# Kernel optimization log

Hardware: AMD Instinct MI355X
Metric: run time of the kernel (lower is better)

The kernel has to match this reference:

```python
import jax, jax.numpy as jnp
import numpy as np

B, T, C = 4, 2048, 2048
H = 16
D = C // H  # 128


def setup_inputs() -> dict:
    key = jax.random.key(0)
    k1, k2, k3, k4 = jax.random.split(key, 4)
    x = jax.random.normal(k1, (B, T, C), dtype=jnp.float32)
    rope_freqs = jax.random.uniform(k2, (D // 2,), dtype=jnp.float32)
    # torch Linear weights: (out_features, in_features)
    W_attn = jax.random.normal(k3, (3 * C, C), dtype=jnp.float32) * (1.0 / np.sqrt(C))
    W_proj = jax.random.normal(k4, (C, C), dtype=jnp.float32) * (1.0 / np.sqrt(C))
    return {"x": x, "rope_freqs": rope_freqs, "W_attn": W_attn, "W_proj": W_proj}


def _apply_rope(q, k, rope_freqs):
    # q, k: (B, H, T, D); rope_freqs: (D//2,)
    S = q.shape[2]
    positions = jnp.arange(S, dtype=q.dtype)[:, None]            # (S, 1)
    theta = positions * rope_freqs[None, :]                       # (S, D//2)
    sin_t = jnp.sin(theta)[None, None]                            # (1,1,S,D//2)
    cos_t = jnp.cos(theta)[None, None]
    q1, q2 = q[..., 0::2], q[..., 1::2]
    k1, k2 = k[..., 0::2], k[..., 1::2]
    q_out = jnp.concatenate([q1 * cos_t - q2 * sin_t, q1 * sin_t + q2 * cos_t], axis=-1)
    k_out = jnp.concatenate([k1 * cos_t - k2 * sin_t, k1 * sin_t + k2 * cos_t], axis=-1)
    return q_out, k_out


def reference(x, rope_freqs, W_attn, W_proj):
    b, t, c = x.shape
    qkv = jnp.einsum('btc,fc->btf', x, W_attn)                    # (B,T,3C)
    q, k, v = jnp.split(qkv, 3, axis=-1)
    q = q.reshape(b, t, H, D).transpose(0, 2, 1, 3)               # (B,H,T,D)
    k = k.reshape(b, t, H, D).transpose(0, 2, 1, 3)
    v = v.reshape(b, t, H, D).transpose(0, 2, 1, 3)
    q, k = _apply_rope(q, k, rope_freqs)
    scale = 1.0 / jnp.sqrt(jnp.asarray(D, dtype=x.dtype))
    scores = jnp.einsum('bhqd,bhkd->bhqk', q, k) * scale          # (B,H,T,T)
    causal = jnp.tril(jnp.ones((t, t), dtype=bool))
    scores = jnp.where(causal[None, None], scores, jnp.asarray(-jnp.inf, dtype=scores.dtype))
    probs = jax.nn.softmax(scores, axis=-1)
    y = jnp.einsum('bhqk,bhkd->bhqd', probs, v)                   # (B,H,T,D)
    y = y.transpose(0, 2, 1, 3).reshape(b, t, c)
    return jnp.einsum('btc,fc->btf', y, W_proj)
```

## Files before the change

kernel.cpp:

```cpp
#include <hip/hip_runtime.h>
#include <cstdint>
#include <cstddef>


typedef unsigned short u16;
typedef u16    u16x8 __attribute__((ext_vector_type(8)));
typedef __bf16 bf16x8 __attribute__((ext_vector_type(8)));
typedef float  f32x4 __attribute__((ext_vector_type(4)));

#define MFMA16(a, b, c) __builtin_amdgcn_mfma_f32_16x16x32_bf16( \
    __builtin_bit_cast(bf16x8, (a)), __builtin_bit_cast(bf16x8, (b)), (c), 0, 0, 0)

static __device__ __forceinline__ u16 f2b(float f) {
  unsigned u = __builtin_bit_cast(unsigned, f);
  unsigned r = (u + 0x7FFFu + ((u >> 16) & 1u)) >> 16;
  return (u16)r;
}

static __device__ __forceinline__ void gld_lds16(const void* g, void* l) {
  __builtin_amdgcn_global_load_lds(
      (__attribute__((address_space(1))) unsigned int*)(void*)(g),
      (__attribute__((address_space(3))) unsigned int*)(l),
      16, 0, 0);
}

#define BARRIER() asm volatile("s_barrier" ::: "memory")
#define LGKM0()   do { asm volatile("s_waitcnt lgkmcnt(0)" ::: "memory"); \
                       __builtin_amdgcn_sched_barrier(0); } while (0)
#define WAIT_VM(n) asm volatile("s_waitcnt vmcnt(" #n ")" ::: "memory")

__global__ __launch_bounds__(256) void cvt_bf16(const float4* __restrict__ src,
                                                u16x8* __restrict__ dst, int n8) {
  int i = blockIdx.x * 256 + threadIdx.x;
  if (i >= n8) return;
  float4 a = src[i * 2], b = src[i * 2 + 1];
  u16x8 o;
  o[0] = f2b(a.x); o[1] = f2b(a.y); o[2] = f2b(a.z); o[3] = f2b(a.w);
  o[4] = f2b(b.x); o[5] = f2b(b.y); o[6] = f2b(b.z); o[7] = f2b(b.w);
  dst[i] = o;
}

static __device__ __forceinline__ void rdA(u16x8 (&af)[4][2], const u16* p,
                                           int cx0, int cx1) {
#pragma unroll
  for (int i = 0; i < 4; ++i) {
    af[i][0] = *(const u16x8*)(p + i * 1024 + cx0);
    af[i][1] = *(const u16x8*)(p + i * 1024 + cx1);
  }
}

static __device__ __forceinline__ void rdB(u16x8 (&bf)[2][2], const u16* p,
                                           int cx0, int cx1) {
#pragma unroll
  for (int j = 0; j < 2; ++j) {
    bf[j][0] = *(const u16x8*)(p + j * 1024 + cx0);
    bf[j][1] = *(const u16x8*)(p + j * 1024 + cx1);
  }
}

static __device__ __forceinline__ void mm16(f32x4 (&acc)[8][4], int ib, int jb,
                                            const u16x8 (&af)[4][2],
                                            const u16x8 (&bf)[2][2]) {
#pragma unroll
  for (int i = 0; i < 4; ++i)
#pragma unroll
    for (int j = 0; j < 2; ++j) {
      acc[ib + i][jb + j] = MFMA16(af[i][0], bf[j][0], acc[ib + i][jb + j]);
      acc[ib + i][jb + j] = MFMA16(af[i][1], bf[j][1], acc[ib + i][jb + j]);
    }
}

static __device__ __forceinline__ void gemm256_main(
    const u16* __restrict__ A, const u16* __restrict__ Bw, int K,
    int m0, int n0, u16* sm, f32x4 (&acc)[8][4]) {
  const int tid = threadIdx.x;
  const int lane = tid & 63, wv = tid >> 6;
  const int quad = lane >> 4, col = lane & 15;
  const int wm = wv >> 2, wn = wv & 3;

  u16* LA0 = sm;
  u16* LB0 = sm + 16384;
  u16* LA1 = sm + 32768;
  u16* LB1 = sm + 49152;

#pragma unroll
  for (int i = 0; i < 8; ++i)
#pragma unroll
    for (int j = 0; j < 4; ++j) acc[i][j] = (f32x4){0.f, 0.f, 0.f, 0.f};

  const int r8 = lane >> 3, ch = lane & 7;
  const int sc8 = (ch ^ r8) << 3;
  const u16 *aS[4], *bS[4];
  int dof[4];
#pragma unroll
  for (int u = 0; u < 4; ++u) {
    int row = u * 64 + wv * 8 + r8;
    aS[u] = A + (size_t)(m0 + row) * K + sc8;
    bS[u] = Bw + (size_t)(n0 + row) * K + sc8;
    dof[u] = (u * 64 + wv * 8) * 64;
  }

  const int cx0 = ((quad) ^ (col & 7)) << 3;
  const int cx1 = ((4 | quad) ^ (col & 7)) << 3;
  const int offA = (wm * 128 + col) * 64;
  const int offB = (wn * 64 + col) * 64;

  gld_lds16(bS[0], LB0 + dof[0]); gld_lds16(bS[1], LB0 + dof[1]);
  gld_lds16(bS[2], LB0 + dof[2]); gld_lds16(bS[3], LB0 + dof[3]);
  gld_lds16(aS[0], LA0 + dof[0]); gld_lds16(aS[2], LA0 + dof[2]);
  gld_lds16(aS[1], LA0 + dof[1]); gld_lds16(aS[3], LA0 + dof[3]);
  WAIT_VM(2);
  BARRIER();

  u16x8 af[4][2], bfL[2][2], bfH[2][2];
  const int nIt = K >> 7;
#pragma unroll 1
  for (int it = 0; it < nIt; ++it) {
    const size_t ko = (size_t)it * 128 + 64;
    const size_t kn = (size_t)it * 128 + 128;
    const bool hn = (it + 1 < nIt);

    rdA(af, LA0 + offA, cx0, cx1);
    rdB(bfL, LB0 + offB, cx0, cx1);
    gld_lds16(bS[0] + ko, LB1 + dof[0]); gld_lds16(bS[1] + ko, LB1 + dof[1]);
    BARRIER(); LGKM0();
    __builtin_amdgcn_s_setprio(1); mm16(acc, 0, 0, af, bfL);
    __builtin_amdgcn_s_setprio(0);
    BARRIER();
    rdB(bfH, LB0 + offB + 2048, cx0, cx1);
    gld_lds16(bS[2] + ko, LB1 + dof[2]); gld_lds16(bS[3] + ko, LB1 + dof[3]);
    WAIT_VM(4);
    BARRIER(); LGKM0();
    __builtin_amdgcn_s_setprio(1); mm16(acc, 0, 2, af, bfH);
    __builtin_amdgcn_s_setprio(0);
    BARRIER();
    rdA(af, LA0 + offA + 4096, cx0, cx1);
    gld_lds16(aS[0] + ko, LA1 + dof[0]); gld_lds16(aS[2] + ko, LA1 + dof[2]);
    BARRIER(); LGKM0();
    __builtin_amdgcn_s_setprio(1); mm16(acc, 4, 0, af, bfL);
    __builtin_amdgcn_s_setprio(0);
    BARRIER();
    gld_lds16(aS[1] + ko, LA1 + dof[1]); gld_lds16(aS[3] + ko, LA1 + dof[3]);
    WAIT_VM(2);
    BARRIER(); __builtin_amdgcn_sched_barrier(0);
    __builtin_amdgcn_s_setprio(1); mm16(acc, 4, 2, af, bfH);
    __builtin_amdgcn_s_setprio(0);
    BARRIER();
    rdA(af, LA1 + offA, cx0, cx1);
    rdB(bfL, LB1 + offB, cx0, cx1);
    if (hn) { gld_lds16(bS[0] + kn, LB0 + dof[0]); gld_lds16(bS[1] + kn, LB0 + dof[1]); }
    BARRIER(); LGKM0();
    __builtin_amdgcn_s_setprio(1); mm16(acc, 0, 0, af, bfL);
    __builtin_amdgcn_s_setprio(0);
    BARRIER();
    rdB(bfH, LB1 + offB + 2048, cx0, cx1);
    if (hn) {
      gld_lds16(bS[2] + kn, LB0 + dof[2]); gld_lds16(bS[3] + kn, LB0 + dof[3]);
      WAIT_VM(4);
    } else {
      WAIT_VM(0);
    }
    BARRIER(); LGKM0();
    __builtin_amdgcn_s_setprio(1); mm16(acc, 0, 2, af, bfH);
    __builtin_amdgcn_s_setprio(0);
    BARRIER();
    rdA(af, LA1 + offA + 4096, cx0, cx1);
    if (hn) { gld_lds16(aS[0] + kn, LA0 + dof[0]); gld_lds16(aS[2] + kn, LA0 + dof[2]); }
    BARRIER(); LGKM0();
    __builtin_amdgcn_s_setprio(1); mm16(acc, 4, 0, af, bfL);
    __builtin_amdgcn_s_setprio(0);
    BARRIER();
    if (hn) { gld_lds16(aS[1] + kn, LA0 + dof[1]); gld_lds16(aS[3] + kn, LA0 + dof[3]); }
    WAIT_VM(2);
    BARRIER(); __builtin_amdgcn_sched_barrier(0);
    __builtin_amdgcn_s_setprio(1); mm16(acc, 4, 2, af, bfH);
    __builtin_amdgcn_s_setprio(0);
    BARRIER();
  }
}

__global__ __launch_bounds__(512, 2) void gemm_qkv(
    const u16* __restrict__ A, const u16* __restrict__ Bw,
    const float* __restrict__ freqs, int K,
    u16* __restrict__ Qp, u16* __restrict__ Kp, u16* __restrict__ Vp) {
  extern __shared__ u16 sm[];
  const int m0 = blockIdx.y * 256, n0 = blockIdx.x * 256;
  f32x4 acc[8][4];
  gemm256_main(A, Bw, K, m0, n0, sm, acc);

  const int tid = threadIdx.x;
  const int lane = tid & 63, wv = tid >> 6;
  const int quad = lane >> 4, col = lane & 15;
  const int wm = wv >> 2, wn = wv & 3;

  const int which = n0 >> 11;
  if (which == 2) {
#pragma unroll
    for (int i = 0; i < 8; ++i) {
      int mg = m0 + wm * 128 + i * 16 + quad * 4;
#pragma unroll
      for (int j = 0; j < 4; ++j) {
        int vcol = (n0 + wn * 64 + j * 16 + col) & 2047;
        int h = vcol >> 7, d = vcol & 127;
#pragma unroll
        for (int r = 0; r < 4; ++r) {
          int m = mg + r;
          int b = m >> 11, t = m & 2047;
          size_t off = ((((size_t)(b * 16 + h)) * 32 + (size_t)(t >> 6)) * 128 + (size_t)d) * 64
                       + (size_t)(t & 63);
          Vp[off] = f2b(acc[i][j][r]);
        }
      }
    }
  } else {
    u16* dst = (which == 0) ? Qp : Kp;
#pragma unroll
    for (int j = 0; j < 4; ++j) {
      int ncol = (n0 + wn * 64 + j * 16 + col) & 2047;
      int h = ncol >> 7, dd = ncol & 127;
      int jj = dd >> 1;
      bool even = (dd & 1) == 0;
      float fr = freqs[jj];
      int dout = even ? jj : jj + 64;
#pragma unroll
      for (int i = 0; i < 8; ++i) {
        int mg = m0 + wm * 128 + i * 16 + quad * 4;
#pragma unroll
        for (int r = 0; r < 4; ++r) {
          float own = acc[i][j][r];
          float par = __shfl_xor(own, 1);
          int m = mg + r;
          int b = m >> 11, t = m & 2047;
          float theta = (float)t * fr;
          float rev = theta * 0.15915494309189535f;
          rev -= floorf(rev);
          float s = __builtin_amdgcn_sinf(rev);
          float c = __builtin_amdgcn_cosf(rev);
          float outv = even ? (own * c - par * s) : (par * s + own * c);
          size_t off = ((((size_t)(b * 16 + h)) << 11 | (size_t)t) << 7) | (size_t)dout;
          dst[off] = f2b(outv);
        }
      }
    }
  }
}

__global__ __launch_bounds__(512, 2) void gemm_proj(
    const u16* __restrict__ A, const u16* __restrict__ Bw,
    int N, int K, float* __restrict__ out) {
  extern __shared__ u16 sm[];
  const int m0 = blockIdx.y * 256, n0 = blockIdx.x * 256;
  f32x4 acc[8][4];
  gemm256_main(A, Bw, K, m0, n0, sm, acc);

  const int tid = threadIdx.x;
  const int lane = tid & 63, wv = tid >> 6;
  const int quad = lane >> 4, col = lane & 15;
  const int wm = wv >> 2, wn = wv & 3;

#pragma unroll
  for (int i = 0; i < 8; ++i) {
    int mg = m0 + wm * 128 + i * 16 + quad * 4;
#pragma unroll
    for (int j = 0; j < 4; ++j) {
      int ng = n0 + wn * 64 + j * 16 + col;
#pragma unroll
      for (int r = 0; r < 4; ++r) out[(size_t)(mg + r) * N + ng] = acc[i][j][r];
    }
  }
}

__global__ __launch_bounds__(512, 4) void fattn(
    const u16* __restrict__ Qb, const u16* __restrict__ Kb, const u16* __restrict__ Vt,
    u16* __restrict__ Yb) {
  __shared__ alignas(16) u16 lK[64 * 128];
  __shared__ alignas(16) u16 lVt[128 * 64];
  __shared__ alignas(16) u16 lP[8][16 * 64];

  const int tid = threadIdx.x;
  const int lane = tid & 63, wv = tid >> 6;
  const int quad = lane >> 4, col = lane & 15;
  const int bh = blockIdx.x;
  const int p = blockIdx.y;
  const int b = bh >> 4, h = bh & 15;
  const size_t base = (size_t)bh << 18;
  const float kcomb = 0.08838834764831845f * 1.4426950408889634f;

#pragma unroll 1
  for (int phase = 0; phase < 2; ++phase) {
    const int tq = phase ? (15 - p) : p;
    const int qr0 = tq * 128 + wv * 16;
    const int dkt = qr0 >> 6;

    u16x8 qf[4];
#pragma unroll
    for (int t = 0; t < 4; ++t)
      qf[t] = *(const u16x8*)(Qb + base + (size_t)(qr0 + col) * 128 + t * 32 + quad * 8);

    f32x4 mrow = (f32x4){-1e30f, -1e30f, -1e30f, -1e30f};
    f32x4 lrow = (f32x4){0.f, 0.f, 0.f, 0.f};
    f32x4 o[8];
#pragma unroll
    for (int dt = 0; dt < 8; ++dt) o[dt] = (f32x4){0.f, 0.f, 0.f, 0.f};

    const int nkt = 2 * tq + 2;
#pragma unroll 1
    for (int kt = 0; kt < nkt; ++kt) {
      __syncthreads();
      if (wv < 4) {
#pragma unroll
        for (int u = 0; u < 4; ++u) {
          int row = wv * 16 + u * 4 + (lane >> 4);
          int sc = (lane & 15) ^ (row & 15);
          gld_lds16(Kb + base + (size_t)(kt * 64 + row) * 128 + (sc << 3),
                    lK + (size_t)(wv * 16 + u * 4) * 128);
        }
      } else {
        int vw = wv - 4;
        const u16* vbase = Vt + ((size_t)(bh * 32 + kt) << 13);
#pragma unroll
        for (int u = 0; u < 4; ++u) {
          int row = vw * 32 + u * 8 + (lane >> 3);
          int sc = (lane & 7) ^ (row & 7);
          gld_lds16(vbase + (size_t)row * 64 + (sc << 3),
                    lVt + (size_t)(vw * 32 + u * 8) * 64);
        }
      }
      __syncthreads();

      if (kt <= dkt) {
        f32x4 sv[4];
#pragma unroll
        for (int nt = 0; nt < 4; ++nt) {
          f32x4 s = (f32x4){0.f, 0.f, 0.f, 0.f};
#pragma unroll
          for (int t = 0; t < 4; ++t) {
            int krow = nt * 16 + col;
            u16x8 kf = *(const u16x8*)&lK[krow * 128 + ((((t << 2) | quad) ^ (krow & 15)) << 3)];
            s = MFMA16(qf[t], kf, s);
          }
          sv[nt] = s;
        }
#pragma unroll
        for (int nt = 0; nt < 4; ++nt)
#pragma unroll
          for (int r = 0; r < 4; ++r) sv[nt][r] *= kcomb;
        if (kt == dkt) {
#pragma unroll
          for (int nt = 0; nt < 4; ++nt) {
            int cg = kt * 64 + nt * 16 + col;
#pragma unroll
            for (int r = 0; r < 4; ++r)
              if (cg > qr0 + quad * 4 + r) sv[nt][r] = -1e30f;
          }
        }
        f32x4 mx = sv[0];
#pragma unroll
        for (int nt = 1; nt < 4; ++nt)
#pragma unroll
          for (int r = 0; r < 4; ++r) mx[r] = fmaxf(mx[r], sv[nt][r]);
#pragma unroll
        for (int off = 1; off < 16; off <<= 1)
#pragma unroll
          for (int r = 0; r < 4; ++r) mx[r] = fmaxf(mx[r], __shfl_xor(mx[r], off));
        f32x4 alpha;
#pragma unroll
        for (int r = 0; r < 4; ++r) {
          float mn = fmaxf(mrow[r], mx[r]);
          alpha[r] = exp2f(mrow[r] - mn);
          mrow[r] = mn;
        }
        f32x4 ps = (f32x4){0.f, 0.f, 0.f, 0.f};
#pragma unroll
        for (int nt = 0; nt < 4; ++nt)
#pragma unroll
          for (int r = 0; r < 4; ++r) {
            float pe = exp2f(sv[nt][r] - mrow[r]);
            ps[r] += pe;
            int row = quad * 4 + r;
            int ch = ((nt << 1) | (col >> 3)) ^ (row & 7);
            lP[wv][row * 64 + (ch << 3) + (col & 7)] = f2b(pe);
          }
#pragma unroll
        for (int off = 1; off < 16; off <<= 1)
#pragma unroll
          for (int r = 0; r < 4; ++r) ps[r] += __shfl_xor(ps[r], off);
#pragma unroll
        for (int r = 0; r < 4; ++r) lrow[r] = lrow[r] * alpha[r] + ps[r];
#pragma unroll
        for (int dt = 0; dt < 8; ++dt)
#pragma unroll
          for (int r = 0; r < 4; ++r) o[dt][r] *= alpha[r];
#pragma unroll
        for (int t = 0; t < 2; ++t) {
          u16x8 pf = *(const u16x8*)&lP[wv][col * 64 + ((((t << 2) | quad) ^ (col & 7)) << 3)];
#pragma unroll
          for (int dt = 0; dt < 8; ++dt) {
            int drow = dt * 16 + col;
            u16x8 vf = *(const u16x8*)&lVt[drow * 64 + ((((t << 2) | quad) ^ (drow & 7)) << 3)];
            o[dt] = MFMA16(pf, vf, o[dt]);
          }
        }
      }
    }

    f32x4 inv;
#pragma unroll
    for (int r = 0; r < 4; ++r) inv[r] = 1.0f / lrow[r];
#pragma unroll
    for (int dt = 0; dt < 8; ++dt)
#pragma unroll
      for (int r = 0; r < 4; ++r) {
        float y = o[dt][r] * inv[r];
        int q = qr0 + quad * 4 + r;
        Yb[((size_t)(b * 2048 + q)) * 2048 + h * 128 + dt * 16 + col] = f2b(y);
      }
  }
}

extern "C" void kernel_launch(void* const* d_in, const int* in_sizes, int n_in,
                              void* d_out, int out_size, void* d_ws, size_t ws_size,
                              hipStream_t stream) {
  (void)in_sizes; (void)n_in; (void)out_size; (void)ws_size;
  const float* x     = (const float*)d_in[0];
  const float* freqs = (const float*)d_in[1];
  const float* Wattn = (const float*)d_in[2];
  const float* Wproj = (const float*)d_in[3];
  float* out = (float*)d_out;
  char* ws = (char*)d_ws;

  u16* Wq_b = (u16*)(ws + 0);
  u16* Wp_b = (u16*)(ws + 25165824);
  u16* x_b  = (u16*)(ws + 33554432);
  u16* Qb   = (u16*)(ws + 67108864);
  u16* Kb   = (u16*)(ws + 100663296);
  u16* Vt   = (u16*)(ws + 134217728);
  u16* Yb   = (u16*)(ws + 167772160);

  static bool attr_done = false;
  if (!attr_done) {
    (void)hipFuncSetAttribute((const void*)gemm_qkv,
                              hipFuncAttributeMaxDynamicSharedMemorySize, 131072);
    (void)hipFuncSetAttribute((const void*)gemm_proj,
                              hipFuncAttributeMaxDynamicSharedMemorySize, 131072);
    attr_done = true;
  }

  cvt_bf16<<<6144, 256, 0, stream>>>((const float4*)Wattn, (u16x8*)Wq_b, 12582912 / 8);
  cvt_bf16<<<2048, 256, 0, stream>>>((const float4*)Wproj, (u16x8*)Wp_b, 4194304 / 8);
  cvt_bf16<<<8192, 256, 0, stream>>>((const float4*)x, (u16x8*)x_b, 16777216 / 8);

  gemm_qkv<<<dim3(24, 32), 512, 131072, stream>>>(x_b, Wq_b, freqs, 2048, Qb, Kb, Vt);
  fattn<<<dim3(64, 8), 512, 0, stream>>>(Qb, Kb, Vt, Yb);
  gemm_proj<<<dim3(8, 32), 512, 131072, stream>>>(Yb, Wp_b, 2048, 2048, out);
}
```

Before: 591.0 us.

## Stage GEMM epilogues through LDS, remap block order, double-buffer attention K/V loads

The QKV GEMM epilogue now writes RoPE'd Q/K and transposed V tiles into swizzled LDS and then stores them with coalesced 16-byte global writes, in place of scattered 2-byte stores. Both GEMMs use a 1D grid with a remapped block order, likely to improve L2 reuse across the XCDs. Flash attention double-buffers its K/V tiles in dynamic LDS so the next tile's loads overlap compute. In exchange it uses more LDS and adds barriers, which may lower attention occupancy.

```diff
diff --git a/kernel.cpp b/kernel.cpp
--- a/kernel.cpp
+++ b/kernel.cpp
@@ -184,7 +184,12 @@
     const float* __restrict__ freqs, int K,
     u16* __restrict__ Qp, u16* __restrict__ Kp, u16* __restrict__ Vp) {
   extern __shared__ u16 sm[];
-  const int m0 = blockIdx.y * 256, n0 = blockIdx.x * 256;
+  const int bid = blockIdx.x;
+  const int x = bid & 7, o = bid >> 3;
+  const int rnd = o >> 5, w = o & 31;
+  const int m0 = (x * 4 + (w & 3)) * 256;
+  const int n0 = (rnd * 8 + (w >> 2)) * 256;
+
   f32x4 acc[8][4];
   gemm256_main(A, Bw, K, m0, n0, sm, acc);
 
@@ -194,53 +199,86 @@
   const int wm = wv >> 2, wn = wv & 3;
 
   const int which = n0 >> 11;
+  const int h0 = (n0 & 2047) >> 7;
+  const int b = m0 >> 11, t0 = m0 & 2047;
+  const int hl = wn >> 1;
+
+  __syncthreads();
+
   if (which == 2) {
 #pragma unroll
-    for (int i = 0; i < 8; ++i) {
-      int mg = m0 + wm * 128 + i * 16 + quad * 4;
-#pragma unroll
-      for (int j = 0; j < 4; ++j) {
-        int vcol = (n0 + wn * 64 + j * 16 + col) & 2047;
-        int h = vcol >> 7, d = vcol & 127;
+    for (int j = 0; j < 4; ++j) {
+      int d = (wn & 1) * 64 + j * 16 + col;
+      int key = (d >> 1) & 7;
+#pragma unroll
+      for (int i = 0; i < 8; ++i)
 #pragma unroll
         for (int r = 0; r < 4; ++r) {
-          int m = mg + r;
-          int b = m >> 11, t = m & 2047;
-          size_t off = ((((size_t)(b * 16 + h)) * 32 + (size_t)(t >> 6)) * 128 + (size_t)d) * 64
-                       + (size_t)(t & 63);
-          Vp[off] = f2b(acc[i][j][r]);
+          int tgl = wm * 128 + i * 16 + quad * 4 + r;
+          int reg = hl * 4 + (tgl >> 6);
+          int tc = tgl & 63;
+          sm[reg * 8192 + d * 64 + (((tc >> 3) ^ key) << 3) + (tc & 7)] =
+              f2b(acc[i][j][r]);
         }
-      }
+    }
+    __syncthreads();
+#pragma unroll
+    for (int s = 0; s < 16; ++s) {
+      int cch = tid + (s << 9);
+      int reg = cch >> 10, ci = cch & 1023;
+      int d = ci >> 3, cc = ci & 7;
+      u16x8 v = *(const u16x8*)(sm + reg * 8192 + d * 64 +
+                                (((cc ^ ((d >> 1) & 7))) << 3));
+      int hh = reg >> 2, ktg = reg & 3;
+      int kt = (t0 >> 6) + ktg;
+      size_t off = (((size_t)((b * 16 + h0 + hh) * 32 + kt)) << 13) +
+                   (size_t)d * 64 + (cc << 3);
+      *(u16x8*)(Vp + off) = v;
     }
   } else {
     u16* dst = (which == 0) ? Qp : Kp;
+    const bool evenlane = (col & 1) == 0;
+    const int rlo = evenlane ? 0 : 2;
 #pragma unroll
     for (int j = 0; j < 4; ++j) {
-      int ncol = (n0 + wn * 64 + j * 16 + col) & 2047;
-      int h = ncol >> 7, dd = ncol & 127;
+      int dd = (wn & 1) * 64 + j * 16 + col;
       int jj = dd >> 1;
-      bool even = (dd & 1) == 0;
       float fr = freqs[jj];
-      int dout = even ? jj : jj + 64;
 #pragma unroll
       for (int i = 0; i < 8; ++i) {
-        int mg = m0 + wm * 128 + i * 16 + quad * 4;
-#pragma unroll
-        for (int r = 0; r < 4; ++r) {
-          float own = acc[i][j][r];
-          float par = __shfl_xor(own, 1);
-          int m = mg + r;
-          int b = m >> 11, t = m & 2047;
+        float oth[4];
+#pragma unroll
+        for (int r = 0; r < 4; ++r) oth[r] = __shfl_xor(acc[i][j][r], 1);
+#pragma unroll
+        for (int rr = 0; rr < 2; ++rr) {
+          int r = rlo + rr;
+          float q1 = evenlane ? acc[i][j][r] : oth[r];
+          float q2 = evenlane ? oth[r] : acc[i][j][r];
+          int tgl = wm * 128 + i * 16 + quad * 4 + r;
+          int t = t0 + tgl;
           float theta = (float)t * fr;
           float rev = theta * 0.15915494309189535f;
           rev -= floorf(rev);
-          float s = __builtin_amdgcn_sinf(rev);
-          float c = __builtin_amdgcn_cosf(rev);
-          float outv = even ? (own * c - par * s) : (par * s + own * c);
-          size_t off = ((((size_t)(b * 16 + h)) << 11 | (size_t)t) << 7) | (size_t)dout;
-          dst[off] = f2b(outv);
+          float sn = __builtin_amdgcn_sinf(rev);
+          float cs = __builtin_amdgcn_cosf(rev);
+          unsigned pk = (unsigned)f2b(q1 * cs - q2 * sn) |
+                        ((unsigned)f2b(q1 * sn + q2 * cs) << 16);
+          int row = hl * 256 + tgl;
+          int sc = (jj >> 2) ^ (row & 15);
+          *(unsigned*)(sm + row * 128 + (sc << 3) + 2 * (jj & 3)) = pk;
         }
       }
+    }
+    __syncthreads();
+#pragma unroll
+    for (int s = 0; s < 16; ++s) {
+      int cch = tid + (s << 9);
+      int row = cch >> 4, cc = cch & 15;
+      u16x8 v = *(const u16x8*)(sm + row * 128 + ((cc ^ (row & 15)) << 3));
+      int hh = row >> 8, tl = row & 255;
+      size_t off = ((size_t)((b * 16 + h0 + hh) * 2048 + t0 + tl)) * 128 +
+                   (cc << 3);
+      *(u16x8*)(dst + off) = v;
     }
   }
 }
@@ -249,7 +287,11 @@
     const u16* __restrict__ A, const u16* __restrict__ Bw,
     int N, int K, float* __restrict__ out) {
   extern __shared__ u16 sm[];
-  const int m0 = blockIdx.y * 256, n0 = blockIdx.x * 256;
+  const int bid = blockIdx.x;
+  const int x = bid & 7, w = bid >> 3;
+  const int m0 = (x * 4 + (w & 3)) * 256;
+  const int n0 = (w >> 2) * 256;
+
   f32x4 acc[8][4];
   gemm256_main(A, Bw, K, m0, n0, sm, acc);
 
@@ -273,9 +315,8 @@
 __global__ __launch_bounds__(512, 4) void fattn(
     const u16* __restrict__ Qb, const u16* __restrict__ Kb, const u16* __restrict__ Vt,
     u16* __restrict__ Yb) {
-  __shared__ alignas(16) u16 lK[64 * 128];
-  __shared__ alignas(16) u16 lVt[128 * 64];
-  __shared__ alignas(16) u16 lP[8][16 * 64];
+  extern __shared__ u16 smem[];
+  u16* lP = smem + 32768 + (threadIdx.x >> 6) * 1024;
 
   const int tid = threadIdx.x;
   const int lane = tid & 63, wv = tid >> 6;
@@ -304,31 +345,50 @@
     for (int dt = 0; dt < 8; ++dt) o[dt] = (f32x4){0.f, 0.f, 0.f, 0.f};
 
     const int nkt = 2 * tq + 2;
+
+#define FA_STAGE(KT, BI)                                                        \
+    do {                                                                        \
+      if (wv < 4) {                                                             \
+        u16* lkd = smem + (BI) * 8192;                                          \
+        _Pragma("unroll")                                                       \
+        for (int u = 0; u < 4; ++u) {                                           \
+          int row = wv * 16 + u * 4 + (lane >> 4);                              \
+          int sc = (lane & 15) ^ (row & 15);                                    \
+          gld_lds16(Kb + base + (size_t)((KT) * 64 + row) * 128 + (sc << 3),    \
+                    lkd + (size_t)(wv * 16 + u * 4) * 128);                     \
+        }                                                                       \
+      } else {                                                                  \
+        int vw = wv - 4;                                                        \
+        u16* lvd = smem + 16384 + (BI) * 8192;                                  \
+        const u16* vbase = Vt + ((size_t)(bh * 32 + (KT)) << 13);               \
+        _Pragma("unroll")                                                       \
+        for (int u = 0; u < 4; ++u) {                                           \
+          int row = vw * 32 + u * 8 + (lane >> 3);                              \
+          int sc = (lane & 7) ^ (row & 7);                                      \
+          gld_lds16(vbase + (size_t)row * 64 + (sc << 3),                       \
+                    lvd + (size_t)(vw * 32 + u * 8) * 64);                      \
+        }                                                                       \
+      }                                                                         \
+    } while (0)
+
+    FA_STAGE(0, 0);
+    WAIT_VM(0);
+    BARRIER();
+
 #pragma unroll 1
     for (int kt = 0; kt < nkt; ++kt) {
-      __syncthreads();
-      if (wv < 4) {
-#pragma unroll
-        for (int u = 0; u < 4; ++u) {
-          int row = wv * 16 + u * 4 + (lane >> 4);
-          int sc = (lane & 15) ^ (row & 15);
-          gld_lds16(Kb + base + (size_t)(kt * 64 + row) * 128 + (sc << 3),
-                    lK + (size_t)(wv * 16 + u * 4) * 128);
-        }
+      const int cur = kt & 1;
+      if (kt + 1 < nkt) {
+        FA_STAGE(kt + 1, cur ^ 1);
+        WAIT_VM(4);
       } else {
-        int vw = wv - 4;
-        const u16* vbase = Vt + ((size_t)(bh * 32 + kt) << 13);
-#pragma unroll
-        for (int u = 0; u < 4; ++u) {
-          int row = vw * 32 + u * 8 + (lane >> 3);
-          int sc = (lane & 7) ^ (row & 7);
-          gld_lds16(vbase + (size_t)row * 64 + (sc << 3),
-                    lVt + (size_t)(vw * 32 + u * 8) * 64);
-        }
+        WAIT_VM(0);
       }
-      __syncthreads();
+      BARRIER();
 
       if (kt <= dkt) {
+        const u16* lK = smem + cur * 8192;
+        const u16* lVt = smem + 16384 + cur * 8192;
         f32x4 sv[4];
 #pragma unroll
         for (int nt = 0; nt < 4; ++nt) {
@@ -378,8 +438,8 @@
             float pe = exp2f(sv[nt][r] - mrow[r]);
             ps[r] += pe;
             int row = quad * 4 + r;
-            int ch = ((nt << 1) | (col >> 3)) ^ (row & 7);
-            lP[wv][row * 64 + (ch << 3) + (col & 7)] = f2b(pe);
+            int chn = ((nt << 1) | (col >> 3)) ^ (row & 7);
+            lP[row * 64 + (chn << 3) + (col & 7)] = f2b(pe);
           }
 #pragma unroll
         for (int off = 1; off < 16; off <<= 1)
@@ -393,7 +453,7 @@
           for (int r = 0; r < 4; ++r) o[dt][r] *= alpha[r];
 #pragma unroll
         for (int t = 0; t < 2; ++t) {
-          u16x8 pf = *(const u16x8*)&lP[wv][col * 64 + ((((t << 2) | quad) ^ (col & 7)) << 3)];
+          u16x8 pf = *(const u16x8*)&lP[col * 64 + ((((t << 2) | quad) ^ (col & 7)) << 3)];
 #pragma unroll
           for (int dt = 0; dt < 8; ++dt) {
             int drow = dt * 16 + col;
@@ -402,6 +462,7 @@
           }
         }
       }
+      BARRIER();
     }
 
     f32x4 inv;
@@ -416,6 +477,7 @@
         Yb[((size_t)(b * 2048 + q)) * 2048 + h * 128 + dt * 16 + col] = f2b(y);
       }
   }
+#undef FA_STAGE
 }
 
 extern "C" void kernel_launch(void* const* d_in, const int* in_sizes, int n_in,
@@ -443,6 +505,8 @@
                               hipFuncAttributeMaxDynamicSharedMemorySize, 131072);
     (void)hipFuncSetAttribute((const void*)gemm_proj,
                               hipFuncAttributeMaxDynamicSharedMemorySize, 131072);
+    (void)hipFuncSetAttribute((const void*)fattn,
+                              hipFuncAttributeMaxDynamicSharedMemorySize, 81920);
     attr_done = true;
   }
 
@@ -450,7 +514,7 @@
   cvt_bf16<<<2048, 256, 0, stream>>>((const float4*)Wproj, (u16x8*)Wp_b, 4194304 / 8);
   cvt_bf16<<<8192, 256, 0, stream>>>((const float4*)x, (u16x8*)x_b, 16777216 / 8);
 
-  gemm_qkv<<<dim3(24, 32), 512, 131072, stream>>>(x_b, Wq_b, freqs, 2048, Qb, Kb, Vt);
-  fattn<<<dim3(64, 8), 512, 0, stream>>>(Qb, Kb, Vt, Yb);
-  gemm_proj<<<dim3(8, 32), 512, 131072, stream>>>(Yb, Wp_b, 2048, 2048, out);
-}
+  gemm_qkv<<<dim3(768), 512, 131072, stream>>>(x_b, Wq_b, freqs, 2048, Qb, Kb, Vt);
+  fattn<<<dim3(64, 8), 512, 81920, stream>>>(Qb, Kb, Vt, Yb);
+  gemm_proj<<<dim3(256), 512, 131072, stream>>>(Yb, Wp_b, 2048, 2048, out);
+}
```

Result: slower. 606.5 us (+2.6%).
